# Optimization experiments

Measured on AMD Instinct MI355X. Metric: run time of the kernel, lower is better.

## Reference

```python
import jax, jax.numpy as jnp
import numpy as np

SCOPE = 63
STD = 2.0


def _mexican_hat(scope: int, std: float) -> np.ndarray:
    # Ricker wavelet sampled symmetrically around 0 (semlc weight_initialization.mexican_hat)
    x = np.arange(scope, dtype=np.float64) - scope // 2
    norm = 2.0 / (np.sqrt(3.0 * std) * np.pi ** 0.25)
    w = norm * (1.0 - (x / std) ** 2) * np.exp(-(x ** 2) / (2.0 * std ** 2))
    return w.astype(np.float32)


def setup_inputs() -> dict:
    key = jax.random.key(0)
    activations = jax.random.normal(key, (64, 64, 128, SCOPE), dtype=jnp.float32)
    inhibition_filter = jnp.asarray(_mexican_hat(SCOPE, STD))
    return {"activations": activations, "inhibition_filter": inhibition_filter}


def reference(activations, inhibition_filter):
    # kronecker delta: 1 at index 0, zeros elsewhere
    delta = jnp.zeros((SCOPE,), dtype=activations.dtype).at[0].set(1.0)
    # full (two-sided) 1D FFT along the last axis, complex divide, inverse FFT
    fa = jnp.fft.fft(activations, axis=-1)            # [N, C, H, scope] complex64
    ff = jnp.fft.fft(delta - inhibition_filter)       # [scope] complex64
    out = jnp.fft.ifft(fa / ff, axis=-1)
    # torch.irfft(..., onesided=False) returns the real part of the inverse transform
    return jnp.real(out)
```

## Files before the change

kernel.cpp:

```cpp
#include <hip/hip_runtime.h>
#include <hip/hip_bf16.h>

#define SCOPE 63
#define BT 256
#define RPB 64
#define TILE_ELEMS (RPB * SCOPE)

typedef __attribute__((ext_vector_type(8))) __bf16 v8bf;
typedef __attribute__((ext_vector_type(4))) float f32x4;

#define GLL(gp, lp) __builtin_amdgcn_global_load_lds(                         \
    (const __attribute__((address_space(1))) void*)(gp),                      \
    (__attribute__((address_space(3))) void*)(lp), 16, 0, 0)

#define WS_BHI_OFF 256
#define WS_BLO_OFF 8448

__global__ void compute_inverse_filter(const float* __restrict__ f,
                                       float* __restrict__ ws) {
    __shared__ double cd[SCOPE];
    __shared__ double sd[SCOPE];
    __shared__ double hre[SCOPE];
    __shared__ double him[SCOPE];
    __shared__ float gsm[SCOPE];
    const double TWO_PI = 6.283185307179586476925286766559;
    int t = threadIdx.x;

    if (t < SCOPE) {
        double ang = -TWO_PI * (double)t / (double)SCOPE;
        cd[t] = cos(ang);
        sd[t] = sin(ang);
    }
    __syncthreads();

    if (t < SCOPE) {
        double re = 0.0, im = 0.0;
        for (int n = 0; n < SCOPE; ++n) {
            double x = (n == 0 ? 1.0 : 0.0) - (double)f[n];
            int m = (t * n) % SCOPE;
            re += x * cd[m];
            im += x * sd[m];
        }
        double d = re * re + im * im;
        hre[t] = re / d;
        him[t] = -im / d;
    }
    __syncthreads();

    if (t < SCOPE) {
        double acc = 0.0;
        for (int k = 0; k < SCOPE; ++k) {
            int m = (k * t) % SCOPE;
            acc += hre[k] * cd[m] + him[k] * sd[m];
        }
        float gv = (float)(acc / (double)SCOPE);
        ws[t] = gv;
        gsm[t] = gv;
    }
    __syncthreads();

    __bf16* Bhi = (__bf16*)((char*)ws + WS_BHI_OFF);
    __bf16* Blo = (__bf16*)((char*)ws + WS_BLO_OFF);
    for (int fidx = t; fidx < 4096; fidx += blockDim.x) {
        const int j  = fidx & 7;
        const int fl = (fidx >> 3) & 63;
        const int kt = (fidx >> 9) & 1;
        const int nt = fidx >> 10;
        const int k  = 8 * (fl >> 4) + j + 32 * kt;
        const int n  = 16 * nt + (fl & 15);
        float v = (k < SCOPE && n < SCOPE) ? gsm[(n - k + SCOPE) % SCOPE] : 0.0f;
        __bf16 h = (__bf16)v;
        Bhi[fidx] = h;
        Blo[fidx] = (__bf16)(v - (float)h);
    }
}

__global__ void __launch_bounds__(BT)
circ_conv_kernel(const float* __restrict__ A,
                 const float* __restrict__ WS,
                 float* __restrict__ O) {
    __shared__ __align__(16) float tile[TILE_ELEMS + 16];

    const int tid = threadIdx.x;
    const int w   = tid >> 6;
    const int l   = tid & 63;
    const int c   = l & 15;
    const int q   = l >> 4;

    const long long row0 = (long long)blockIdx.x * RPB;
    const float* __restrict__ src = A + row0 * SCOPE;
    float* __restrict__ dst       = O + row0 * SCOPE;

    const float4* src4 = (const float4*)src;
    float4* w4 = (float4*)tile;
#pragma unroll
    for (int it = 0; it < 3; ++it)
        GLL(src4 + it * 256 + tid, w4 + it * 256 + tid);
    if (tid < 240)
        GLL(src4 + 768 + tid, w4 + 768 + tid);
    if (tid < 16) tile[TILE_ELEMS + tid] = 0.0f;

    const v8bf* BH = (const v8bf*)((const char*)WS + WS_BHI_OFF);
    const v8bf* BL = (const v8bf*)((const char*)WS + WS_BLO_OFF);
    v8bf bh[4][2], bl[4][2];
#pragma unroll
    for (int nt = 0; nt < 4; ++nt)
#pragma unroll
        for (int kt = 0; kt < 2; ++kt) {
            bh[nt][kt] = BH[(nt * 2 + kt) * 64 + l];
            bl[nt][kt] = BL[(nt * 2 + kt) * 64 + l];
        }

    __syncthreads();

    v8bf ah[2], al[2];
#pragma unroll
    for (int kt = 0; kt < 2; ++kt) {
        const float* ap = tile + (16 * w + c) * SCOPE + 8 * q + 32 * kt;
#pragma unroll
        for (int j = 0; j < 8; ++j) {
            float v = ap[j];
            __bf16 h = (__bf16)v;
            ah[kt][j] = h;
            al[kt][j] = (__bf16)(v - (float)h);
        }
    }

#pragma unroll
    for (int nt = 0; nt < 4; ++nt) {
        f32x4 acc = {0.f, 0.f, 0.f, 0.f};
#pragma unroll
        for (int kt = 0; kt < 2; ++kt) {
            acc = __builtin_amdgcn_mfma_f32_16x16x32_bf16(ah[kt], bh[nt][kt], acc, 0, 0, 0);
            acc = __builtin_amdgcn_mfma_f32_16x16x32_bf16(ah[kt], bl[nt][kt], acc, 0, 0, 0);
            acc = __builtin_amdgcn_mfma_f32_16x16x32_bf16(al[kt], bh[nt][kt], acc, 0, 0, 0);
        }
        const int col = 16 * nt + c;
        if (col < SCOPE) {
            float* cp = tile + (16 * w + 4 * q) * SCOPE + col;
#pragma unroll
            for (int i = 0; i < 4; ++i)
                cp[i * SCOPE] = acc[i];
        }
    }

    __syncthreads();

    float4* dst4 = (float4*)dst;
#pragma unroll
    for (int it = 0; it < 3; ++it)
        dst4[it * 256 + tid] = w4[it * 256 + tid];
    if (tid < 240)
        dst4[768 + tid] = w4[768 + tid];
}

extern "C" void kernel_launch(void* const* d_in, const int* in_sizes, int n_in,
                              void* d_out, int out_size, void* d_ws, size_t ws_size,
                              hipStream_t stream) {
    const float* activations = (const float*)d_in[0];
    const float* filt        = (const float*)d_in[1];
    float* out               = (float*)d_out;
    float* ws                = (float*)d_ws;

    hipLaunchKernelGGL(compute_inverse_filter, dim3(1), dim3(BT), 0, stream,
                       filt, ws);

    const long long total = (long long)in_sizes[0];
    const long long rows  = total / SCOPE;
    const int blocks      = (int)(rows / RPB);

    hipLaunchKernelGGL(circ_conv_kernel, dim3(blocks), dim3(BT), 0,
                       stream, activations, ws, out);
}
```

Measured before the change: 57.20 us.

## Swizzle LDS tile rows to 64 floats and drop block-wide output barrier

```diff
diff --git a/kernel.cpp b/kernel.cpp
--- a/kernel.cpp
+++ b/kernel.cpp
@@ -4,7 +4,6 @@
 #define SCOPE 63
 #define BT 256
 #define RPB 64
-#define TILE_ELEMS (RPB * SCOPE)
 
 typedef __attribute__((ext_vector_type(8))) __bf16 v8bf;
 typedef __attribute__((ext_vector_type(4))) float f32x4;
@@ -79,7 +78,7 @@
 circ_conv_kernel(const float* __restrict__ A,
                  const float* __restrict__ WS,
                  float* __restrict__ O) {
-    __shared__ __align__(16) float tile[TILE_ELEMS + 16];
+    __shared__ __align__(16) unsigned char tile[16384 + 16];
 
     const int tid = threadIdx.x;
     const int w   = tid >> 6;
@@ -91,14 +90,23 @@
     const float* __restrict__ src = A + row0 * SCOPE;
     float* __restrict__ dst       = O + row0 * SCOPE;
 
-    const float4* src4 = (const float4*)src;
-    float4* w4 = (float4*)tile;
+    const bool last = ((int)blockIdx.x == (int)gridDim.x - 1);
+
 #pragma unroll
-    for (int it = 0; it < 3; ++it)
-        GLL(src4 + it * 256 + tid, w4 + it * 256 + tid);
-    if (tid < 240)
-        GLL(src4 + 768 + tid, w4 + 768 + tid);
-    if (tid < 16) tile[TILE_ELEMS + tid] = 0.0f;
+    for (int it = 0; it < 4; ++it) {
+        const int i  = it * 256 + tid;
+        const int r  = i >> 4;
+        const int gl = i & 15;
+        const int gk = gl ^ (r & 7);
+        const bool oob = (gk == 15) && last && (r == 63);
+        if (!oob)
+            GLL(src + r * SCOPE + 4 * gk, tile + i * 16);
+    }
+    if (last && tid < 4) {
+        const int r = 63, gl = 15 ^ (r & 7);
+        float v = (tid < 3) ? src[r * SCOPE + 60 + tid] : 0.0f;
+        *(float*)(tile + r * 256 + gl * 16 + tid * 4) = v;
+    }
 
     const v8bf* BH = (const v8bf*)((const char*)WS + WS_BHI_OFF);
     const v8bf* BL = (const v8bf*)((const char*)WS + WS_BLO_OFF);
@@ -113,19 +121,25 @@
 
     __syncthreads();
 
+    const int r  = 16 * w + c;
+    const int rx = r & 7;
     v8bf ah[2], al[2];
 #pragma unroll
     for (int kt = 0; kt < 2; ++kt) {
-        const float* ap = tile + (16 * w + c) * SCOPE + 8 * q + 32 * kt;
+        const int fg0 = 8 * kt + 2 * q;
+        float4 v0 = *(const float4*)(tile + r * 256 + ((fg0 ^ rx) << 4));
+        float4 v1 = *(const float4*)(tile + r * 256 + (((fg0 + 1) ^ rx) << 4));
+        float tmp[8] = {v0.x, v0.y, v0.z, v0.w, v1.x, v1.y, v1.z, v1.w};
 #pragma unroll
         for (int j = 0; j < 8; ++j) {
-            float v = ap[j];
+            float v = tmp[j];
             __bf16 h = (__bf16)v;
             ah[kt][j] = h;
             al[kt][j] = (__bf16)(v - (float)h);
         }
     }
 
+    float* cw = (float*)(tile + w * 4096);
 #pragma unroll
     for (int nt = 0; nt < 4; ++nt) {
         f32x4 acc = {0.f, 0.f, 0.f, 0.f};
@@ -137,21 +151,22 @@
         }
         const int col = 16 * nt + c;
         if (col < SCOPE) {
-            float* cp = tile + (16 * w + 4 * q) * SCOPE + col;
+            float* cp = cw + (4 * q) * SCOPE + col;
 #pragma unroll
             for (int i = 0; i < 4; ++i)
                 cp[i * SCOPE] = acc[i];
         }
     }
 
-    __syncthreads();
-
-    float4* dst4 = (float4*)dst;
+    float* wdst = dst + (long long)w * (16 * SCOPE);
 #pragma unroll
-    for (int it = 0; it < 3; ++it)
-        dst4[it * 256 + tid] = w4[it * 256 + tid];
-    if (tid < 240)
-        dst4[768 + tid] = w4[768 + tid];
+    for (int it = 0; it < 4; ++it) {
+        const int gidx = it * 64 + l;
+        if (gidx < 252) {
+            float4 v = *(const float4*)(tile + w * 4096 + gidx * 16);
+            *(float4*)(wdst + gidx * 4) = v;
+        }
+    }
 }
 
 extern "C" void kernel_launch(void* const* d_in, const int* in_sizes, int n_in,
```

New measurement: 57.67 us. No clear change (+0.8%).
